# Performance work log

Hardware: AMD Instinct MI355X
Metric: run time of the kernel (lower is better)

## Reference

```python
import jax, jax.numpy as jnp
import numpy as np

D_MODEL = 1024
NUM_HEADS = 16
HEAD_DIM = D_MODEL // NUM_HEADS


def setup_inputs() -> dict:
    key = jax.random.key(0)
    ks = jax.random.split(key, 9)
    s = D_MODEL ** -0.5  # roughly like nn.Linear init scale
    x = jax.random.normal(ks[0], (4, 2048, D_MODEL), dtype=jnp.float32)
    Wq = jax.random.normal(ks[1], (D_MODEL, D_MODEL), dtype=jnp.float32) * s
    bq = jax.random.normal(ks[2], (D_MODEL,), dtype=jnp.float32) * s
    Wk = jax.random.normal(ks[3], (D_MODEL, D_MODEL), dtype=jnp.float32) * s
    bk = jax.random.normal(ks[4], (D_MODEL,), dtype=jnp.float32) * s
    Wv = jax.random.normal(ks[5], (D_MODEL, D_MODEL), dtype=jnp.float32) * s
    bv = jax.random.normal(ks[6], (D_MODEL,), dtype=jnp.float32) * s
    Wo = jax.random.normal(ks[7], (D_MODEL, D_MODEL), dtype=jnp.float32) * s
    bo = jax.random.normal(ks[8], (D_MODEL,), dtype=jnp.float32) * s
    return {"x": x, "Wq": Wq, "bq": bq, "Wk": Wk, "bk": bk,
            "Wv": Wv, "bv": bv, "Wo": Wo, "bo": bo}


def reference(x, Wq, bq, Wk, bk, Wv, bv, Wo, bo):
    B, S, D = x.shape
    H, Dh = NUM_HEADS, HEAD_DIM
    scale = Dh ** -0.5
    # nn.Linear: x @ W.T + b
    q = (x @ Wq.T + bq).reshape(B, S, H, Dh)
    k = (x @ Wk.T + bk).reshape(B, S, H, Dh)
    v = (x @ Wv.T + bv).reshape(B, S, H, Dh)
    # scores: (B, H, S, S), full materialization as in the original bmm path
    dp = scale * jnp.einsum('bqhd,bkhd->bhqk', q, k)
    att = jax.nn.softmax(dp, axis=-1)
    out = jnp.einsum('bhqk,bkhd->bqhd', att, v).reshape(B, S, D)
    return out @ Wo.T + bo
```

## Files before the change

### kernel.cpp

```cpp
#include <hip/hip_runtime.h>
#include <stdint.h>

typedef __attribute__((ext_vector_type(8))) __bf16 bf16x8;
typedef __attribute__((ext_vector_type(4))) float floatx4;

#define DEV __device__ __forceinline__

DEV unsigned short f2bf(float f) {
    union { float f; unsigned u; } uf; uf.f = f;
    unsigned u = uf.u;
    unsigned r = (u + 0x7fffu + ((u >> 16) & 1u)) >> 16;
    return (unsigned short)r;
}

DEV float fast_exp2(float x) {
#if __has_builtin(__builtin_amdgcn_exp2f)
    return __builtin_amdgcn_exp2f(x);
#else
    return exp2f(x);
#endif
}

DEV unsigned pack_trunc2(float lo, float hi) {
    return __builtin_amdgcn_perm(__float_as_uint(hi), __float_as_uint(lo), 0x07060302u);
}

DEV void async16(const void* g, void* l) {
    __builtin_amdgcn_global_load_lds(
        (const __attribute__((address_space(1))) void*)g,
        (__attribute__((address_space(3))) void*)l, 16, 0, 0);
}

__global__ void cast_all_kernel(const float* __restrict__ x,
                                const float* __restrict__ Wq, const float* __restrict__ Wk,
                                const float* __restrict__ Wv, const float* __restrict__ Wo,
                                const float* __restrict__ bq, const float* __restrict__ bk,
                                const float* __restrict__ bv,
                                unsigned short* __restrict__ xb,
                                unsigned short* __restrict__ wqkv,
                                unsigned short* __restrict__ wo,
                                float* __restrict__ bqkv) {
    const int NX = 2097152;
    const int NW = 262144;
    int i = blockIdx.x * blockDim.x + threadIdx.x;
    if (i < NX) {
        float4 v = reinterpret_cast<const float4*>(x)[i];
        ushort4 o;
        o.x = f2bf(v.x); o.y = f2bf(v.y); o.z = f2bf(v.z); o.w = f2bf(v.w);
        reinterpret_cast<ushort4*>(xb)[i] = o;
        return;
    }
    int j = i - NX;
    if (j < 4 * NW) {
        int seg = j >> 18, off = j & (NW - 1);
        const float* src = (seg == 0) ? Wq : (seg == 1) ? Wk : (seg == 2) ? Wv : Wo;
        unsigned short* dst = (seg < 3) ? (wqkv + seg * 1048576) : wo;
        float4 v = reinterpret_cast<const float4*>(src)[off];
        ushort4 o;
        o.x = f2bf(v.x); o.y = f2bf(v.y); o.z = f2bf(v.z); o.w = f2bf(v.w);
        reinterpret_cast<ushort4*>(dst)[off] = o;
        return;
    }
    int k = j - 4 * NW;
    if (k < 768) {
        int seg = k >> 8, off = k & 255;
        const float* src = (seg == 0) ? bq : (seg == 1) ? bk : bv;
        reinterpret_cast<float4*>(bqkv)[k] = reinterpret_cast<const float4*>(src)[off];
    }
}

template <int MODE>
__global__ __launch_bounds__(256)
void gemm128(const unsigned short* __restrict__ A,
             const unsigned short* __restrict__ B,
             const float* __restrict__ bias,
             unsigned short* __restrict__ q_ws,
             unsigned short* __restrict__ k_ws,
             unsigned short* __restrict__ v_ws,
             float* __restrict__ fout) {
    constexpr int K = 1024;
    __shared__ alignas(16) unsigned short smem[128 * 136];
    unsigned short* sA = smem;
    unsigned short* sB = smem + 128 * 64;
    unsigned short* sT = smem;

    const int tid = threadIdx.x;
    const int w = tid >> 6, lane = tid & 63, quad = lane >> 4, l16 = lane & 15;
    const int wr = w >> 1, wc = w & 1;
    const int bm = blockIdx.x, bn = blockIdx.y;
    const int arow0 = bm * 128, brow0 = bn * 128;

    floatx4 acc[4][4];
#pragma unroll
    for (int i = 0; i < 4; i++)
#pragma unroll
        for (int j = 0; j < 4; j++) acc[i][j] = (floatx4){0.f, 0.f, 0.f, 0.f};

    for (int k0 = 0; k0 < K; k0 += 64) {
#pragma unroll
        for (int i = 0; i < 4; i++) {
            int cb = i * 256 + w * 64;
            int ci = cb + lane;
            int row = ci >> 3, cl = ci & 7, cs = cl ^ (row & 7);
            async16(A + (size_t)(arow0 + row) * K + k0 + cs * 8, (char*)sA + cb * 16);
            async16(B + (size_t)(brow0 + row) * K + k0 + cs * 8, (char*)sB + cb * 16);
        }
        __syncthreads();
#pragma unroll
        for (int kk = 0; kk < 2; kk++) {
            bf16x8 aF[4], bF[4];
#pragma unroll
            for (int i = 0; i < 4; i++) {
                int row = wr * 64 + i * 16 + l16;
                int c = kk * 4 + quad, ph = c ^ (row & 7);
                aF[i] = *reinterpret_cast<const bf16x8*>(sA + row * 64 + ph * 8);
            }
#pragma unroll
            for (int j = 0; j < 4; j++) {
                int row = wc * 64 + j * 16 + l16;
                int c = kk * 4 + quad, ph = c ^ (row & 7);
                bF[j] = *reinterpret_cast<const bf16x8*>(sB + row * 64 + ph * 8);
            }
#pragma unroll
            for (int i = 0; i < 4; i++)
#pragma unroll
                for (int j = 0; j < 4; j++)
                    acc[i][j] = __builtin_amdgcn_mfma_f32_16x16x32_bf16(
                        aF[i], bF[j], acc[i][j], 0, 0, 0);
        }
        __syncthreads();
    }

    if (bn < 16) {
        unsigned short* dst = (bn < 8) ? q_ws : k_ws;
        const float sc = (bn < 8) ? 0.18033688f : 1.0f;
#pragma unroll
        for (int j = 0; j < 4; j++) {
            const int c = wc * 64 + j * 16 + l16;
            const float bia = bias[brow0 + c];
#pragma unroll
            for (int i = 0; i < 4; i++) {
                int s_loc = wr * 64 + i * 16 + quad * 4;
#pragma unroll
                for (int r = 0; r < 4; r++)
                    sT[(s_loc + r) * 136 + c] = f2bf((acc[i][j][r] + bia) * sc);
            }
        }
        __syncthreads();
        const int nnbase = (bn & 7) * 128;
        const int c0 = (tid & 15) * 8;
        const int h = (nnbase + c0) >> 6, d = c0 & 63;
#pragma unroll
        for (int it = 0; it < 8; it++) {
            int s_loc = (tid >> 4) + it * 16;
            int s = arow0 + s_loc;
            int bb = s >> 11, s4 = s & 2047;
            uint4 vdat = *reinterpret_cast<const uint4*>(sT + s_loc * 136 + c0);
            *reinterpret_cast<uint4*>(
                dst + ((size_t)(bb * 16 + h) * 2048 + s4) * 64 + d) = vdat;
        }
    } else {
#pragma unroll
        for (int j = 0; j < 4; j++) {
            const int c = wc * 64 + j * 16 + l16;
            const float bia = bias[brow0 + c];
#pragma unroll
            for (int i = 0; i < 4; i++) {
#pragma unroll
                for (int r = 0; r < 4; r++) {
                    int v = wr * 64 + (quad * 4 + r) * 4 + i;
                    sT[c * 136 + v] = f2bf(acc[i][j][r] + bia);
                }
            }
        }
        __syncthreads();
        const int bb = bm >> 4, blk = bm & 15;
        const int chunk = tid & 15;
#pragma unroll
        for (int it = 0; it < 8; it++) {
            int row = (tid >> 4) + it * 16;
            int h = (bn - 16) * 2 + (row >> 6), d = row & 63;
            ushort4 lo = *reinterpret_cast<const ushort4*>(sT + row * 136 + chunk * 8);
            ushort4 hi = *reinterpret_cast<const ushort4*>(sT + row * 136 + chunk * 8 + 4);
            size_t off = ((size_t)(bb * 16 + h) * 64 + d) * 2048 + blk * 128 + chunk * 8;
            *reinterpret_cast<ushort4*>(v_ws + off) = lo;
            *reinterpret_cast<ushort4*>(v_ws + off + 4) = hi;
        }
    }
}

__global__ __launch_bounds__(256)
void gemm_oproj(const unsigned short* __restrict__ A,
                const unsigned short* __restrict__ Bw,
                const float* __restrict__ bias,
                float* __restrict__ fout) {
    constexpr int K = 1024;
    __shared__ alignas(16) unsigned short smem[192 * 64];
    unsigned short* sA = smem;
    unsigned short* sB = smem + 128 * 64;
    float* sT32 = reinterpret_cast<float*>(smem);

    const int tid = threadIdx.x;
    const int w = tid >> 6, lane = tid & 63, quad = lane >> 4, l16 = lane & 15;
    const int wr = w >> 1, wc = w & 1;
    const int bm = blockIdx.x, bn = blockIdx.y;
    const int arow0 = bm * 128, brow0 = bn * 64;

    floatx4 acc[4][2];
#pragma unroll
    for (int i = 0; i < 4; i++)
#pragma unroll
        for (int j = 0; j < 2; j++) acc[i][j] = (floatx4){0.f, 0.f, 0.f, 0.f};

    for (int k0 = 0; k0 < K; k0 += 64) {
#pragma unroll
        for (int i = 0; i < 4; i++) {
            int ci = i * 256 + tid;
            int row = ci >> 3, cs = (ci & 7) ^ (row & 7);
            async16(A + (size_t)(arow0 + row) * K + k0 + cs * 8, (char*)sA + ci * 16);
        }
#pragma unroll
        for (int i = 0; i < 2; i++) {
            int ci = i * 256 + tid;
            int row = ci >> 3, cs = (ci & 7) ^ (row & 7);
            async16(Bw + (size_t)(brow0 + row) * K + k0 + cs * 8, (char*)sB + ci * 16);
        }
        __syncthreads();
#pragma unroll
        for (int kk = 0; kk < 2; kk++) {
            bf16x8 aF[4], bF[2];
#pragma unroll
            for (int i = 0; i < 4; i++) {
                int row = wr * 64 + i * 16 + l16;
                int ph = (kk * 4 + quad) ^ (row & 7);
                aF[i] = *reinterpret_cast<const bf16x8*>(sA + row * 64 + ph * 8);
            }
#pragma unroll
            for (int j = 0; j < 2; j++) {
                int row = wc * 32 + j * 16 + l16;
                int ph = (kk * 4 + quad) ^ (row & 7);
                bF[j] = *reinterpret_cast<const bf16x8*>(sB + row * 64 + ph * 8);
            }
#pragma unroll
            for (int i = 0; i < 4; i++)
#pragma unroll
                for (int j = 0; j < 2; j++)
                    acc[i][j] = __builtin_amdgcn_mfma_f32_16x16x32_bf16(
                        aF[i], bF[j], acc[i][j], 0, 0, 0);
        }
        __syncthreads();
    }

#pragma unroll
    for (int ch = 0; ch < 2; ch++) {
        if (ch) __syncthreads();
        if (wr == ch) {
#pragma unroll
            for (int j = 0; j < 2; j++) {
                const int c = wc * 32 + j * 16 + l16;
                const float bia = bias[brow0 + c];
#pragma unroll
                for (int i = 0; i < 4; i++) {
                    int s_loc = i * 16 + quad * 4;
#pragma unroll
                    for (int r = 0; r < 4; r++)
                        sT32[(s_loc + r) * 68 + c] = acc[i][j][r] + bia;
                }
            }
        }
        __syncthreads();
        const int cpos = (tid & 15) * 4;
#pragma unroll
        for (int it = 0; it < 4; it++) {
            int s_loc = (tid >> 4) + it * 16;
            int grow = arow0 + ch * 64 + s_loc;
            float4 vv = *reinterpret_cast<const float4*>(sT32 + s_loc * 68 + cpos);
            *reinterpret_cast<float4*>(fout + (size_t)grow * 1024 + brow0 + cpos) = vv;
        }
    }
}

__global__ __launch_bounds__(256, 4)
void attn_kernel(const unsigned short* __restrict__ q_ws,
                 const unsigned short* __restrict__ k_ws,
                 const unsigned short* __restrict__ v_ws,
                 unsigned short* __restrict__ o_ws) {
    __shared__ alignas(16) unsigned short smem[20480];

    const int tid = threadIdx.x;
    const int w = tid >> 6, lane = tid & 63, quad = lane >> 4, l16 = lane & 15;
    const int id = blockIdx.x;
    const int bh = (id >> 7) * 8 + (id & 7);
    const int q0 = ((id >> 3) & 15) * 128;
    const size_t base = (size_t)bh * 2048 * 64;

    unsigned short* sPw = smem + 16384 + w * 1024;

    bf16x8 aQ[2][2];
#pragma unroll
    for (int g = 0; g < 2; g++) {
        int qrow = q0 + g * 64 + w * 16 + l16;
        const unsigned short* qp = q_ws + base + (size_t)qrow * 64 + quad * 8;
        aQ[g][0] = *reinterpret_cast<const bf16x8*>(qp);
        aQ[g][1] = *reinterpret_cast<const bf16x8*>(qp + 32);
    }

    const unsigned short* kg[2];
    const unsigned short* vg[2];
    int loff[2];
#pragma unroll
    for (int it = 0; it < 2; it++) {
        int ci = it * 256 + tid;
        int row = ci >> 3, cl = ci & 7, cs = cl ^ (row & 7);
        kg[it] = k_ws + base + (size_t)row * 64 + cs * 8;
        vg[it] = v_ws + base + (size_t)row * 2048 + cs * 8;
        loff[it] = ci * 8;
    }

    const __bf16 one = (__bf16)1.0f;
    const bf16x8 vOnes = {one, one, one, one, one, one, one, one};

    floatx4 oAcc[2][4], rsAcc[2];
#pragma unroll
    for (int g = 0; g < 2; g++) {
#pragma unroll
        for (int j = 0; j < 4; j++) oAcc[g][j] = (floatx4){0.f, 0.f, 0.f, 0.f};
        rsAcc[g] = (floatx4){0.f, 0.f, 0.f, 0.f};
    }

    {
#pragma unroll
        for (int it = 0; it < 2; it++) {
            async16(kg[it], smem + loff[it]);
            async16(vg[it], smem + 8192 + loff[it]);
        }
    }

    const int xr = l16 & 7;
    const int offw0 = l16 * 64 + (((2 * quad) ^ xr) << 3);
    const int offw1 = l16 * 64 + (((2 * quad + 1) ^ xr) << 3);
    const int offr0 = l16 * 64 + ((quad ^ xr) << 3);
    const int offr1 = l16 * 64 + (((4 + quad) ^ xr) << 3);

    for (int t = 0; t < 32; t++) {
        const int b = t & 1;
        const unsigned short* sK = smem + b * 4096;
        const unsigned short* sVt = smem + 8192 + b * 4096;
        __syncthreads();

        if (t < 31) {
            const int kv0 = (t + 1) * 64;
            unsigned short* dK = smem + (b ^ 1) * 4096;
            unsigned short* dV = smem + 8192 + (b ^ 1) * 4096;
#pragma unroll
            for (int it = 0; it < 2; it++) {
                async16(kg[it] + (size_t)kv0 * 64, dK + loff[it]);
                async16(vg[it] + kv0, dV + loff[it]);
            }
        }

        floatx4 s0[4], s1[4];
#pragma unroll
        for (int j = 0; j < 4; j++) {
            s0[j] = (floatx4){0.f, 0.f, 0.f, 0.f};
            s1[j] = (floatx4){0.f, 0.f, 0.f, 0.f};
        }
        __builtin_amdgcn_s_setprio(1);
#pragma unroll
        for (int kk = 0; kk < 2; kk++) {
#pragma unroll
            for (int j = 0; j < 4; j++) {
                int krow = j * 16 + l16;
                int ph = (kk * 4 + quad) ^ (krow & 7);
                bf16x8 aK = *reinterpret_cast<const bf16x8*>(sK + krow * 64 + ph * 8);
                s0[j] = __builtin_amdgcn_mfma_f32_16x16x32_bf16(aK, aQ[0][kk], s0[j], 0, 0, 0);
                s1[j] = __builtin_amdgcn_mfma_f32_16x16x32_bf16(aK, aQ[1][kk], s1[j], 0, 0, 0);
            }
        }
        __builtin_amdgcn_s_setprio(0);

#pragma unroll
        for (int j = 0; j < 4; j++)
#pragma unroll
            for (int r = 0; r < 4; r++) s0[j][r] = fast_exp2(s0[j][r]);
        {
            uint4 w0, w1;
            w0.x = pack_trunc2(s0[0][0], s0[1][0]);
            w0.y = pack_trunc2(s0[2][0], s0[3][0]);
            w0.z = pack_trunc2(s0[0][1], s0[1][1]);
            w0.w = pack_trunc2(s0[2][1], s0[3][1]);
            w1.x = pack_trunc2(s0[0][2], s0[1][2]);
            w1.y = pack_trunc2(s0[2][2], s0[3][2]);
            w1.z = pack_trunc2(s0[0][3], s0[1][3]);
            w1.w = pack_trunc2(s0[2][3], s0[3][3]);
            *reinterpret_cast<uint4*>(sPw + offw0) = w0;
            *reinterpret_cast<uint4*>(sPw + offw1) = w1;
        }

        {
            bf16x8 aPa = *reinterpret_cast<const bf16x8*>(sPw + offr0);
            bf16x8 aPb = *reinterpret_cast<const bf16x8*>(sPw + offr1);
            __builtin_amdgcn_s_setprio(1);
#pragma unroll
            for (int jd = 0; jd < 4; jd++) {
                int drow = jd * 16 + l16;
                int ph0 = quad ^ (drow & 7);
                bf16x8 bVa = *reinterpret_cast<const bf16x8*>(sVt + drow * 64 + ph0 * 8);
                oAcc[0][jd] = __builtin_amdgcn_mfma_f32_16x16x32_bf16(aPa, bVa, oAcc[0][jd], 0, 0, 0);
                int ph1 = (4 + quad) ^ (drow & 7);
                bf16x8 bVb = *reinterpret_cast<const bf16x8*>(sVt + drow * 64 + ph1 * 8);
                oAcc[0][jd] = __builtin_amdgcn_mfma_f32_16x16x32_bf16(aPb, bVb, oAcc[0][jd], 0, 0, 0);
            }
            rsAcc[0] = __builtin_amdgcn_mfma_f32_16x16x32_bf16(aPa, vOnes, rsAcc[0], 0, 0, 0);
            rsAcc[0] = __builtin_amdgcn_mfma_f32_16x16x32_bf16(aPb, vOnes, rsAcc[0], 0, 0, 0);
            __builtin_amdgcn_s_setprio(0);
        }

#pragma unroll
        for (int j = 0; j < 4; j++)
#pragma unroll
            for (int r = 0; r < 4; r++) s1[j][r] = fast_exp2(s1[j][r]);
        {
            uint4 w0, w1;
            w0.x = pack_trunc2(s1[0][0], s1[1][0]);
            w0.y = pack_trunc2(s1[2][0], s1[3][0]);
            w0.z = pack_trunc2(s1[0][1], s1[1][1]);
            w0.w = pack_trunc2(s1[2][1], s1[3][1]);
            w1.x = pack_trunc2(s1[0][2], s1[1][2]);
            w1.y = pack_trunc2(s1[2][2], s1[3][2]);
            w1.z = pack_trunc2(s1[0][3], s1[1][3]);
            w1.w = pack_trunc2(s1[2][3], s1[3][3]);
            *reinterpret_cast<uint4*>(sPw + offw0) = w0;
            *reinterpret_cast<uint4*>(sPw + offw1) = w1;
        }

        {
            bf16x8 aPa = *reinterpret_cast<const bf16x8*>(sPw + offr0);
            bf16x8 aPb = *reinterpret_cast<const bf16x8*>(sPw + offr1);
            __builtin_amdgcn_s_setprio(1);
#pragma unroll
            for (int jd = 0; jd < 4; jd++) {
                int drow = jd * 16 + l16;
                int ph0 = quad ^ (drow & 7);
                bf16x8 bVa = *reinterpret_cast<const bf16x8*>(sVt + drow * 64 + ph0 * 8);
                oAcc[1][jd] = __builtin_amdgcn_mfma_f32_16x16x32_bf16(aPa, bVa, oAcc[1][jd], 0, 0, 0);
                int ph1 = (4 + quad) ^ (drow & 7);
                bf16x8 bVb = *reinterpret_cast<const bf16x8*>(sVt + drow * 64 + ph1 * 8);
                oAcc[1][jd] = __builtin_amdgcn_mfma_f32_16x16x32_bf16(aPb, bVb, oAcc[1][jd], 0, 0, 0);
            }
            rsAcc[1] = __builtin_amdgcn_mfma_f32_16x16x32_bf16(aPa, vOnes, rsAcc[1], 0, 0, 0);
            rsAcc[1] = __builtin_amdgcn_mfma_f32_16x16x32_bf16(aPb, vOnes, rsAcc[1], 0, 0, 0);
            __builtin_amdgcn_s_setprio(0);
        }
    }

    const int bb = bh >> 4, h = bh & 15;
#pragma unroll
    for (int g = 0; g < 2; g++) {
        float inv[4];
#pragma unroll
        for (int r = 0; r < 4; r++) inv[r] = 1.0f / rsAcc[g][r];
#pragma unroll
        for (int jd = 0; jd < 4; jd++) {
            int d = jd * 16 + l16;
#pragma unroll
            for (int r = 0; r < 4; r++) {
                int s = q0 + g * 64 + w * 16 + quad * 4 + r;
                float v = oAcc[g][jd][r] * inv[r];
                o_ws[((size_t)bb * 2048 + s) * 1024 + h * 64 + d] = f2bf(v);
            }
        }
    }
}

extern "C" void kernel_launch(void* const* d_in, const int* in_sizes, int n_in,
                              void* d_out, int out_size, void* d_ws, size_t ws_size,
                              hipStream_t stream) {
    const float* x  = (const float*)d_in[0];
    const float* Wq = (const float*)d_in[1];
    const float* bq = (const float*)d_in[2];
    const float* Wk = (const float*)d_in[3];
    const float* bk = (const float*)d_in[4];
    const float* Wv = (const float*)d_in[5];
    const float* bv = (const float*)d_in[6];
    const float* Wo = (const float*)d_in[7];
    const float* bo = (const float*)d_in[8];
    float* out = (float*)d_out;

    char* ws = (char*)d_ws;
    unsigned short* xb   = (unsigned short*)(ws);
    unsigned short* wqkv = (unsigned short*)(ws + (16ull << 20));
    unsigned short* wo   = (unsigned short*)(ws + (22ull << 20));
    float*          bqkv = (float*)(ws + (24ull << 20));
    unsigned short* q_ws = (unsigned short*)(ws + (25ull << 20));
    unsigned short* k_ws = (unsigned short*)(ws + (41ull << 20));
    unsigned short* v_ws = (unsigned short*)(ws + (57ull << 20));
    unsigned short* o_ws = xb;

    cast_all_kernel<<<12291, 256, 0, stream>>>(x, Wq, Wk, Wv, Wo, bq, bk, bv,
                                               xb, wqkv, wo, bqkv);

    gemm128<0><<<dim3(64, 24), 256, 0, stream>>>(xb, wqkv, bqkv, q_ws, k_ws, v_ws, nullptr);
    attn_kernel<<<1024, 256, 0, stream>>>(q_ws, k_ws, v_ws, o_ws);
    gemm_oproj<<<dim3(64, 16), 256, 0, stream>>>(o_ws, wo, bo, out);
}
```

Before: 265.3 us.

## Enlarge QKV projection GEMM tile to 256x128 with 512-thread blocks

The QKV projection GEMM now uses 256x128 output tiles computed by 8 waves in 512-thread blocks, halving the grid along M. Each B (weight) tile loaded into shared memory is reused across twice as many rows, which cuts global and L2 traffic for the weights. The epilogue writes out the two 128-row halves one after the other through the shared staging buffer, at the cost of extra barriers. The grid shrinks to 768 blocks, which may lower occupancy and load balance across CUs.

```diff
diff --git a/kernel.cpp b/kernel.cpp
--- a/kernel.cpp
+++ b/kernel.cpp
@@ -69,26 +69,24 @@
     }
 }
 
-template <int MODE>
-__global__ __launch_bounds__(256)
-void gemm128(const unsigned short* __restrict__ A,
+__global__ __launch_bounds__(512)
+void gemm256(const unsigned short* __restrict__ A,
              const unsigned short* __restrict__ B,
              const float* __restrict__ bias,
              unsigned short* __restrict__ q_ws,
              unsigned short* __restrict__ k_ws,
-             unsigned short* __restrict__ v_ws,
-             float* __restrict__ fout) {
+             unsigned short* __restrict__ v_ws) {
     constexpr int K = 1024;
-    __shared__ alignas(16) unsigned short smem[128 * 136];
+    __shared__ alignas(16) unsigned short smem[24576];
     unsigned short* sA = smem;
-    unsigned short* sB = smem + 128 * 64;
+    unsigned short* sB = smem + 256 * 64;
     unsigned short* sT = smem;
 
     const int tid = threadIdx.x;
     const int w = tid >> 6, lane = tid & 63, quad = lane >> 4, l16 = lane & 15;
     const int wr = w >> 1, wc = w & 1;
     const int bm = blockIdx.x, bn = blockIdx.y;
-    const int arow0 = bm * 128, brow0 = bn * 128;
+    const int arow0 = bm * 256, brow0 = bn * 128;
 
     floatx4 acc[4][4];
 #pragma unroll
@@ -99,11 +97,15 @@
     for (int k0 = 0; k0 < K; k0 += 64) {
 #pragma unroll
         for (int i = 0; i < 4; i++) {
-            int cb = i * 256 + w * 64;
-            int ci = cb + lane;
-            int row = ci >> 3, cl = ci & 7, cs = cl ^ (row & 7);
-            async16(A + (size_t)(arow0 + row) * K + k0 + cs * 8, (char*)sA + cb * 16);
-            async16(B + (size_t)(brow0 + row) * K + k0 + cs * 8, (char*)sB + cb * 16);
+            int ci = i * 512 + tid;
+            int row = ci >> 3, cs = (ci & 7) ^ (row & 7);
+            async16(A + (size_t)(arow0 + row) * K + k0 + cs * 8, (char*)sA + ci * 16);
+        }
+#pragma unroll
+        for (int i = 0; i < 2; i++) {
+            int ci = i * 512 + tid;
+            int row = ci >> 3, cs = (ci & 7) ^ (row & 7);
+            async16(B + (size_t)(brow0 + row) * K + k0 + cs * 8, (char*)sB + ci * 16);
         }
         __syncthreads();
 #pragma unroll
@@ -134,57 +136,72 @@
     if (bn < 16) {
         unsigned short* dst = (bn < 8) ? q_ws : k_ws;
         const float sc = (bn < 8) ? 0.18033688f : 1.0f;
-#pragma unroll
-        for (int j = 0; j < 4; j++) {
-            const int c = wc * 64 + j * 16 + l16;
-            const float bia = bias[brow0 + c];
-#pragma unroll
-            for (int i = 0; i < 4; i++) {
-                int s_loc = wr * 64 + i * 16 + quad * 4;
-#pragma unroll
-                for (int r = 0; r < 4; r++)
-                    sT[(s_loc + r) * 136 + c] = f2bf((acc[i][j][r] + bia) * sc);
-            }
-        }
-        __syncthreads();
         const int nnbase = (bn & 7) * 128;
         const int c0 = (tid & 15) * 8;
         const int h = (nnbase + c0) >> 6, d = c0 & 63;
 #pragma unroll
-        for (int it = 0; it < 8; it++) {
-            int s_loc = (tid >> 4) + it * 16;
-            int s = arow0 + s_loc;
-            int bb = s >> 11, s4 = s & 2047;
-            uint4 vdat = *reinterpret_cast<const uint4*>(sT + s_loc * 136 + c0);
-            *reinterpret_cast<uint4*>(
-                dst + ((size_t)(bb * 16 + h) * 2048 + s4) * 64 + d) = vdat;
+        for (int p = 0; p < 2; p++) {
+            if (p) __syncthreads();
+            if ((wr >> 1) == p) {
+                const int wrl = wr & 1;
+#pragma unroll
+                for (int j = 0; j < 4; j++) {
+                    const int c = wc * 64 + j * 16 + l16;
+                    const float bia = bias[brow0 + c];
+#pragma unroll
+                    for (int i = 0; i < 4; i++) {
+                        int s_loc = wrl * 64 + i * 16 + quad * 4;
+#pragma unroll
+                        for (int r = 0; r < 4; r++)
+                            sT[(s_loc + r) * 136 + c] = f2bf((acc[i][j][r] + bia) * sc);
+                    }
+                }
+            }
+            __syncthreads();
+#pragma unroll
+            for (int it = 0; it < 4; it++) {
+                int s_loc = (tid >> 4) + it * 32;
+                int s = arow0 + p * 128 + s_loc;
+                int bb = s >> 11, s4 = s & 2047;
+                uint4 vdat = *reinterpret_cast<const uint4*>(sT + s_loc * 136 + c0);
+                *reinterpret_cast<uint4*>(
+                    dst + ((size_t)(bb * 16 + h) * 2048 + s4) * 64 + d) = vdat;
+            }
         }
     } else {
-#pragma unroll
-        for (int j = 0; j < 4; j++) {
-            const int c = wc * 64 + j * 16 + l16;
-            const float bia = bias[brow0 + c];
-#pragma unroll
-            for (int i = 0; i < 4; i++) {
-#pragma unroll
-                for (int r = 0; r < 4; r++) {
-                    int v = wr * 64 + (quad * 4 + r) * 4 + i;
-                    sT[c * 136 + v] = f2bf(acc[i][j][r] + bia);
+        const int chunk = tid & 15;
+#pragma unroll
+        for (int p = 0; p < 2; p++) {
+            if (p) __syncthreads();
+            if ((wr >> 1) == p) {
+                const int wrl = wr & 1;
+#pragma unroll
+                for (int j = 0; j < 4; j++) {
+                    const int c = wc * 64 + j * 16 + l16;
+                    const float bia = bias[brow0 + c];
+#pragma unroll
+                    for (int i = 0; i < 4; i++) {
+#pragma unroll
+                        for (int r = 0; r < 4; r++) {
+                            int v = wrl * 64 + (quad * 4 + r) * 4 + i;
+                            sT[c * 136 + v] = f2bf(acc[i][j][r] + bia);
+                        }
+                    }
                 }
             }
-        }
-        __syncthreads();
-        const int bb = bm >> 4, blk = bm & 15;
-        const int chunk = tid & 15;
-#pragma unroll
-        for (int it = 0; it < 8; it++) {
-            int row = (tid >> 4) + it * 16;
-            int h = (bn - 16) * 2 + (row >> 6), d = row & 63;
-            ushort4 lo = *reinterpret_cast<const ushort4*>(sT + row * 136 + chunk * 8);
-            ushort4 hi = *reinterpret_cast<const ushort4*>(sT + row * 136 + chunk * 8 + 4);
-            size_t off = ((size_t)(bb * 16 + h) * 64 + d) * 2048 + blk * 128 + chunk * 8;
-            *reinterpret_cast<ushort4*>(v_ws + off) = lo;
-            *reinterpret_cast<ushort4*>(v_ws + off + 4) = hi;
+            __syncthreads();
+            const int sblk = bm * 2 + p;
+            const int bb2 = sblk >> 4, blk = sblk & 15;
+#pragma unroll
+            for (int it = 0; it < 4; it++) {
+                int row = (tid >> 4) + it * 32;
+                int h = (bn - 16) * 2 + (row >> 6), d = row & 63;
+                ushort4 lo = *reinterpret_cast<const ushort4*>(sT + row * 136 + chunk * 8);
+                ushort4 hi = *reinterpret_cast<const ushort4*>(sT + row * 136 + chunk * 8 + 4);
+                size_t off = ((size_t)(bb2 * 16 + h) * 64 + d) * 2048 + blk * 128 + chunk * 8;
+                *reinterpret_cast<ushort4*>(v_ws + off) = lo;
+                *reinterpret_cast<ushort4*>(v_ws + off + 4) = hi;
+            }
         }
     }
 }
@@ -500,7 +517,7 @@
     cast_all_kernel<<<12291, 256, 0, stream>>>(x, Wq, Wk, Wv, Wo, bq, bk, bv,
                                                xb, wqkv, wo, bqkv);
 
-    gemm128<0><<<dim3(64, 24), 256, 0, stream>>>(xb, wqkv, bqkv, q_ws, k_ws, v_ws, nullptr);
+    gemm256<<<dim3(32, 24), 512, 0, stream>>>(xb, wqkv, bqkv, q_ws, k_ws, v_ws);
     attn_kernel<<<1024, 256, 0, stream>>>(q_ws, k_ws, v_ws, o_ws);
     gemm_oproj<<<dim3(64, 16), 256, 0, stream>>>(o_ws, wo, bo, out);
 }
```

Result: no change. 261.0 us (-1.6%).
